# Performance work log

Hardware: AMD Instinct MI355X
Metric: run time of the kernel (lower is better)

## Reference

```python
import jax, jax.numpy as jnp
import numpy as np

NUM_HEADS = 16
HEAD_DIM = 64
HIDDEN = NUM_HEADS * HEAD_DIM  # 1024
B, S = 2, 2048
INV_NORM = 1.0 / np.sqrt(HEAD_DIM)


def setup_inputs() -> dict:
    key = jax.random.key(0)
    ks = jax.random.split(key, 8)
    hidden_states = jax.random.normal(ks[0], (1, B, S, HIDDEN), dtype=jnp.float32)
    residual = jax.random.normal(ks[1], (B, S, HIDDEN), dtype=jnp.float32)
    # ALiBi bias per (batch*head) broadcast over query positions: [B*H, 1, S]
    slopes = 2.0 ** (-8.0 * (jnp.arange(1, NUM_HEADS + 1, dtype=jnp.float32) / NUM_HEADS))
    pos = jnp.arange(S, dtype=jnp.float32)
    alibi = (slopes[:, None] * pos[None, :])[None]  # [1, H, S]
    alibi = jnp.broadcast_to(alibi, (B, NUM_HEADS, S)).reshape(B * NUM_HEADS, 1, S)
    # causal mask: True = masked out
    attention_mask = jnp.triu(jnp.ones((S, S), dtype=jnp.bool_), k=1)[None, None]  # [1,1,S,S]
    attention_mask = jnp.broadcast_to(attention_mask, (B, 1, S, S))
    W_qkv = jax.random.normal(ks[2], (3 * HIDDEN, HIDDEN), dtype=jnp.float32) * 0.02
    b_qkv = jax.random.normal(ks[3], (3 * HIDDEN,), dtype=jnp.float32) * 0.02
    W_dense = jax.random.normal(ks[4], (HIDDEN, HIDDEN), dtype=jnp.float32) * 0.02
    b_dense = jax.random.normal(ks[5], (HIDDEN,), dtype=jnp.float32) * 0.02
    return {
        "hidden_states": hidden_states,
        "residual": residual,
        "alibi": alibi,
        "attention_mask": attention_mask,
        "W_qkv": W_qkv,
        "b_qkv": b_qkv,
        "W_dense": W_dense,
        "b_dense": b_dense,
    }


def reference(hidden_states, residual, alibi, attention_mask, W_qkv, b_qkv, W_dense, b_dense):
    x = hidden_states[0]  # [B, S, H]
    b, s, _ = x.shape
    fused = x @ W_qkv.T + b_qkv  # [B, S, 3H]
    # Bloom interleaved split: [B, S, nh, 3, hd]
    qkv = fused.reshape(b, s, NUM_HEADS, 3, HEAD_DIM)
    q = jnp.transpose(qkv[..., 0, :], (0, 2, 1, 3))  # [B, nh, S, hd]
    k = jnp.transpose(qkv[..., 1, :], (0, 2, 1, 3))
    v = jnp.transpose(qkv[..., 2, :], (0, 2, 1, 3))
    # baddbmm: alibi + inv_norm * q @ k^T
    scores = jnp.einsum("bhqd,bhkd->bhqk", q, k) * INV_NORM
    scores = scores + alibi.reshape(b, NUM_HEADS, 1, s)  # [B, nh, S, S]
    neg_min = jnp.finfo(scores.dtype).min
    scores = jnp.where(attention_mask, neg_min, scores)
    probs = jax.nn.softmax(scores.astype(jnp.float32), axis=-1).astype(x.dtype)
    ctx = jnp.einsum("bhqk,bhkd->bhqd", probs, v)  # [B, nh, S, hd]
    ctx = jnp.transpose(ctx, (0, 2, 1, 3)).reshape(b, s, HIDDEN)  # merge_heads
    out = ctx @ W_dense.T + b_dense
    return out + residual  # dropout_add, eval mode
```

## Files before the change

kernel.cpp:

```cpp
#include <hip/hip_runtime.h>
#include <hip/hip_bf16.h>

#define NUM_HEADS 16
#define HEAD_DIM  64
#define HIDDEN    1024
#define BATCH     2
#define SEQ       2048
#define K_DIM     1024
#define INV_NORM  0.125f
#define LOG2E     1.4426950408889634f
#define IN2       (INV_NORM * LOG2E)

typedef __attribute__((ext_vector_type(4)))  float f32x4;
typedef __attribute__((ext_vector_type(16))) float f32x16;
typedef __attribute__((ext_vector_type(8)))  short bf16x8;
typedef __attribute__((ext_vector_type(4)))  unsigned int u32x4;
typedef __attribute__((ext_vector_type(2)))  unsigned int u32x2;
typedef unsigned short u16;

__device__ inline u16 f2bf(float f) {
    __hip_bfloat16 h = __float2bfloat16(f);
    return __builtin_bit_cast(u16, h);
}
__device__ inline float bf2f(u16 u) {
    unsigned int v = ((unsigned int)u) << 16;
    return __builtin_bit_cast(float, v);
}

__device__ inline f32x16 mfma32(bf16x8 a, bf16x8 b, f32x16 c) {
    return __builtin_amdgcn_mfma_f32_32x32x16_bf16(a, b, c, 0, 0, 0);
}

__device__ inline void gl_lds16(const u16* g, u16* s) {
    __builtin_amdgcn_global_load_lds(
        (const __attribute__((address_space(1))) unsigned int*)g,
        (__attribute__((address_space(3))) unsigned int*)s, 16, 0, 0);
}

__device__ inline void pack8(const float* src, u16* dst) {
    const float4 v0 = *reinterpret_cast<const float4*>(src);
    const float4 v1 = *reinterpret_cast<const float4*>(src + 4);
    ushort4 o0, o1;
    o0.x = f2bf(v0.x); o0.y = f2bf(v0.y); o0.z = f2bf(v0.z); o0.w = f2bf(v0.w);
    o1.x = f2bf(v1.x); o1.y = f2bf(v1.y); o1.z = f2bf(v1.z); o1.w = f2bf(v1.w);
    *reinterpret_cast<ushort4*>(dst)     = o0;
    *reinterpret_cast<ushort4*>(dst + 4) = o1;
}
__global__ __launch_bounds__(256) void cvt_all(
        const float* __restrict__ x, const float* __restrict__ wq,
        const float* __restrict__ wd,
        u16* __restrict__ xb, u16* __restrict__ wqb, u16* __restrict__ wdb) {
    int t = blockIdx.x * 256 + threadIdx.x;
    if (t < 524288) {
        int mt = t >> 12, rem = t & 4095;
        int kblk = rem >> 6, hf = (rem >> 5) & 1, ra = rem & 31;
        pack8(x + ((size_t)(mt * 32 + ra)) * K_DIM + kblk * 16 + hf * 8,
              xb + (size_t)t * 8);
    } else if (t < 917504) {
        int t2 = t - 524288;
        int nt = t2 >> 12, rem = t2 & 4095;
        int kblk = rem >> 6, hf = (rem >> 5) & 1, ra = rem & 31;
        pack8(wq + ((size_t)(nt * 32 + ra)) * K_DIM + kblk * 16 + hf * 8,
              wqb + (size_t)t2 * 8);
    } else {
        int i = (t - 917504) * 8;
        pack8(wd + i, wdb + i);
    }
}

#define QLOAD(P, kb) {                                                        \
    P##x0 = *reinterpret_cast<const bf16x8*>(pa0 + (size_t)(kb) * 512);       \
    P##x1 = *reinterpret_cast<const bf16x8*>(pa1 + (size_t)(kb) * 512);       \
    P##y0 = *reinterpret_cast<const bf16x8*>(pb0 + (size_t)(kb) * 512);       \
    P##y1 = *reinterpret_cast<const bf16x8*>(pb1 + (size_t)(kb) * 512);       \
    P##x2 = *reinterpret_cast<const bf16x8*>(pa0 + (size_t)(kb + 1) * 512);   \
    P##x3 = *reinterpret_cast<const bf16x8*>(pa1 + (size_t)(kb + 1) * 512);   \
    P##y2 = *reinterpret_cast<const bf16x8*>(pb0 + (size_t)(kb + 1) * 512);   \
    P##y3 = *reinterpret_cast<const bf16x8*>(pb1 + (size_t)(kb + 1) * 512);   \
}
#define QSTEP(P) {                                                            \
    acc[0][0] = mfma32(P##x0, P##y0, acc[0][0]);                              \
    acc[0][1] = mfma32(P##x0, P##y1, acc[0][1]);                              \
    acc[1][0] = mfma32(P##x1, P##y0, acc[1][0]);                              \
    acc[1][1] = mfma32(P##x1, P##y1, acc[1][1]);                              \
    acc[0][0] = mfma32(P##x2, P##y2, acc[0][0]);                              \
    acc[0][1] = mfma32(P##x2, P##y3, acc[0][1]);                              \
    acc[1][0] = mfma32(P##x3, P##y2, acc[1][0]);                              \
    acc[1][1] = mfma32(P##x3, P##y3, acc[1][1]);                              \
}
__global__ __launch_bounds__(256) void gemm_qkv(
        const u16* __restrict__ Af, const u16* __restrict__ Bf,
        const float* __restrict__ bias,
        u16* __restrict__ qo, u16* __restrict__ ko2, u16* __restrict__ vTo) {
    int lin = blockIdx.x;
    int g = lin & 7, i2 = lin >> 3;
    const int mblk = ((g & 3) * 8 + (i2 & 7)) * 128;
    const int nblk = ((g >> 2) * 12 + (i2 >> 3)) * 128;
    const int tid = threadIdx.x;
    const int w = tid >> 6, lane = tid & 63;
    const int la = lane & 31, hi = lane >> 5;
    const int wr = w >> 1, wc = w & 1;
    const int mt0 = (mblk >> 5) + wr * 2;
    const int nt0 = (nblk >> 5) + wc * 2;
    const u16* pa0 = Af + (size_t)mt0 * 64 * 512 + lane * 8;
    const u16* pa1 = pa0 + 64 * 512;
    const u16* pb0 = Bf + (size_t)nt0 * 64 * 512 + lane * 8;
    const u16* pb1 = pb0 + 64 * 512;
    f32x16 acc[2][2] = {};
    bf16x8 ax0, ax1, ax2, ax3, ay0, ay1, ay2, ay3;
    bf16x8 bx0, bx1, bx2, bx3, by0, by1, by2, by3;
    QLOAD(a, 0)
    #pragma unroll 4
    for (int kb = 0; kb < 64; kb += 4) {
        const int n1 = (kb + 2 < 62) ? kb + 2 : 62;
        QLOAD(b, n1)
        QSTEP(a)
        const int n2 = (kb + 4 < 62) ? kb + 4 : 62;
        QLOAD(a, n2)
        QSTEP(b)
    }
    #pragma unroll
    for (int mi = 0; mi < 2; ++mi)
    #pragma unroll
    for (int ni = 0; ni < 2; ++ni) {
        int c = nblk + wc * 64 + ni * 32 + la;
        int h = c / 192, rem = c - h * 192;
        int which = rem >> 6, d = rem & 63;
        float bv = bias[c];
        #pragma unroll
        for (int r = 0; r < 16; ++r) {
            int m = mblk + wr * 64 + mi * 32 + (r & 3) + 8 * (r >> 2) + 4 * hi;
            int bb = m >> 11, s = m & (SEQ - 1);
            int bh = bb * NUM_HEADS + h;
            int t = s >> 5;
            size_t tb = ((size_t)(bh * 64 + t)) * 2048;
            u16 o = f2bf(acc[mi][ni][r] + bv);
            if (which == 2) {
                int dblk = d >> 5, ra = d & 31;
                int k = s & 31, ks = k >> 4, hf = (k >> 3) & 1, e = k & 7;
                vTo[tb + (dblk * 2 + ks) * 512 + hf * 256 + ra * 8 + e] = o;
            } else {
                int kk = d >> 4, hf = (d >> 3) & 1, e = d & 7, ra = s & 31;
                size_t off = tb + kk * 512 + hf * 256 + ra * 8 + e;
                if (which == 0) qo[off] = o;
                else            ko2[off] = o;
            }
        }
    }
}

__global__ __launch_bounds__(256) void gemm_dense(
        const u16* __restrict__ A, const u16* __restrict__ W,
        const float* __restrict__ bias, const float* __restrict__ residual,
        float* __restrict__ out) {
    __shared__ u16 As[64 * 64];
    __shared__ u16 Bs[128 * 64];
    int lin = blockIdx.x;
    int g = lin & 7, i2 = lin >> 3;
    const int mblk = (g * 8 + (i2 & 7)) * 64;
    const int nblk = (i2 >> 3) * 128;
    const int tid = threadIdx.x;
    const int w = tid >> 6, l = tid & 63;
    const int la = l & 31, hi = l >> 5;
    const int wr = w & 1, wc = w >> 1;
    const int kperm = (((l & 7) ^ (l >> 3)) << 3);
    const u16* gA = A + (size_t)(mblk + w * 16 + (l >> 3)) * K_DIM + kperm;
    const u16* gB = W + (size_t)(nblk + w * 32 + (l >> 3)) * K_DIM + kperm;
    const int sca = (la & 7) << 3;
    f32x16 acc2[2] = {};
    for (int kt = 0; kt < 16; ++kt) {
        const int ko = kt * 64;
        gl_lds16(gA + ko,              &As[(w * 16) * 64]);
        gl_lds16(gA + ko + 8 * K_DIM,  &As[(w * 16 + 8) * 64]);
        #pragma unroll
        for (int i = 0; i < 4; ++i)
            gl_lds16(gB + i * 8 * K_DIM + ko, &Bs[(w * 32 + i * 8) * 64]);
        asm volatile("s_waitcnt vmcnt(0)" ::: "memory");
        __syncthreads();
        const u16* pA = &As[(wr * 32 + la) * 64];
        const u16* pB = &Bs[(wc * 64 + la) * 64];
        #pragma unroll
        for (int kk = 0; kk < 4; ++kk) {
            const int co = (kk * 16 + hi * 8) ^ sca;
            bf16x8 a0 = *reinterpret_cast<const bf16x8*>(pA + co);
            bf16x8 b0 = *reinterpret_cast<const bf16x8*>(pB + co);
            bf16x8 b1 = *reinterpret_cast<const bf16x8*>(pB + 32 * 64 + co);
            acc2[0] = mfma32(a0, b0, acc2[0]);
            acc2[1] = mfma32(a0, b1, acc2[1]);
        }
        __syncthreads();
    }
    #pragma unroll
    for (int ni = 0; ni < 2; ++ni) {
        int c = nblk + wc * 64 + ni * 32 + la;
        float bv = bias[c];
        #pragma unroll
        for (int r = 0; r < 16; ++r) {
            int m = mblk + wr * 32 + (r & 3) + 8 * (r >> 2) + 4 * hi;
            out[(size_t)m * HIDDEN + c] = acc2[ni][r] + bv + residual[(size_t)m * HIDDEN + c];
        }
    }
}

__global__ __launch_bounds__(256) void knorm_max(const u16* __restrict__ Kf,
                                                 float* __restrict__ kn,
                                                 unsigned int* __restrict__ ctr) {
    if (blockIdx.x == 0 && threadIdx.x < 8) ctr[threadIdx.x] = 0;
    __shared__ float red[256];
    const int bh = blockIdx.x;
    float mx = 0.f;
    for (int s = threadIdx.x; s < SEQ; s += 256) {
        const u16* kp = Kf + ((size_t)(bh * 64 + (s >> 5))) * 2048 + (s & 31) * 8;
        float ss = 0.f;
        #pragma unroll
        for (int kk = 0; kk < 4; ++kk)
        #pragma unroll
        for (int hf = 0; hf < 2; ++hf) {
            bf16x8 v = *reinterpret_cast<const bf16x8*>(kp + kk * 512 + hf * 256);
            #pragma unroll
            for (int e = 0; e < 8; ++e) {
                float f = bf2f((u16)v[e]);
                ss = fmaf(f, f, ss);
            }
        }
        mx = fmaxf(mx, ss);
    }
    red[threadIdx.x] = mx;
    __syncthreads();
    for (int off = 128; off; off >>= 1) {
        if (threadIdx.x < (unsigned)off)
            red[threadIdx.x] = fmaxf(red[threadIdx.x], red[threadIdx.x + off]);
        __syncthreads();
    }
    if (threadIdx.x == 0) kn[bh] = sqrtf(red[0]);
}

#define LOADT(P, tt) {                                                        \
    const u16* kp_ = kbase + (size_t)(tt) * 2048;                             \
    P##k0 = *reinterpret_cast<const bf16x8*>(kp_);                            \
    P##k1 = *reinterpret_cast<const bf16x8*>(kp_ + 512);                      \
    P##k2 = *reinterpret_cast<const bf16x8*>(kp_ + 1024);                     \
    P##k3 = *reinterpret_cast<const bf16x8*>(kp_ + 1536);                     \
    const u16* vp_ = vbase + (size_t)(tt) * 2048;                             \
    P##v0 = *reinterpret_cast<const bf16x8*>(vp_);                            \
    P##v1 = *reinterpret_cast<const bf16x8*>(vp_ + 512);                      \
    P##v2 = *reinterpret_cast<const bf16x8*>(vp_ + 1024);                     \
    P##v3 = *reinterpret_cast<const bf16x8*>(vp_ + 1536);                     \
}

#define STEP(P, N, tcur, tnxt, DIAG) {                                        \
    f32x16 sca_ = {}, scb_ = {};                                              \
    sca_ = mfma32(P##k0, qf0, sca_);                                          \
    scb_ = mfma32(P##k1, qf1, scb_);                                          \
    sca_ = mfma32(P##k2, qf2, sca_);                                          \
    scb_ = mfma32(P##k3, qf3, scb_);                                          \
    LOADT(N, tnxt)                                                            \
    const float Dt_ = slope2 * (float)((tcur) * 32 - qw);                     \
    float p[16];                                                              \
    _Pragma("unroll")                                                         \
    for (int r = 0; r < 16; ++r)                                              \
        p[r] = __builtin_amdgcn_exp2f(fmaf(sca_[r] + scb_[r], IN2, cl[r] + Dt_)); \
    if (DIAG) {                                                               \
        _Pragma("unroll")                                                     \
        for (int r = 0; r < 16; ++r) {                                        \
            int kr_ = (r & 3) + 8 * (r >> 2) + 4 * hi;                        \
            if (kr_ > la) p[r] = 0.f;                                         \
        }                                                                     \
    }                                                                         \
    l_i += ((p[0] + p[1]) + (p[2] + p[3])) + ((p[4] + p[5]) + (p[6] + p[7]))  \
         + ((p[8] + p[9]) + (p[10] + p[11])) + ((p[12] + p[13]) + (p[14] + p[15])); \
    unsigned pk_[8];                                                          \
    _Pragma("unroll")                                                         \
    for (int m = 0; m < 4; ++m) {                                             \
        unsigned b0_ = __builtin_bit_cast(unsigned, p[4 * m])     + 0x8000u;  \
        unsigned b1_ = __builtin_bit_cast(unsigned, p[4 * m + 1]) + 0x8000u;  \
        unsigned b2_ = __builtin_bit_cast(unsigned, p[4 * m + 2]) + 0x8000u;  \
        unsigned b3_ = __builtin_bit_cast(unsigned, p[4 * m + 3]) + 0x8000u;  \
        pk_[2 * m]     = __builtin_amdgcn_perm(b1_, b0_, 0x07060302u);        \
        pk_[2 * m + 1] = __builtin_amdgcn_perm(b3_, b2_, 0x07060302u);        \
    }                                                                         \
    u32x2 r0_ = __builtin_amdgcn_permlane32_swap(pk_[0], pk_[2], false, false); \
    u32x2 r1_ = __builtin_amdgcn_permlane32_swap(pk_[1], pk_[3], false, false); \
    u32x2 r2_ = __builtin_amdgcn_permlane32_swap(pk_[4], pk_[6], false, false); \
    u32x2 r3_ = __builtin_amdgcn_permlane32_swap(pk_[5], pk_[7], false, false); \
    u32x4 pb0_, pb1_;                                                         \
    pb0_[0] = r0_[0]; pb0_[1] = r1_[0]; pb0_[2] = r0_[1]; pb0_[3] = r1_[1];   \
    pb1_[0] = r2_[0]; pb1_[1] = r3_[0]; pb1_[2] = r2_[1]; pb1_[3] = r3_[1];   \
    bf16x8 pf0_ = __builtin_bit_cast(bf16x8, pb0_);                           \
    bf16x8 pf1_ = __builtin_bit_cast(bf16x8, pb1_);                           \
    o0 = mfma32(P##v0, pf0_, o0);                                             \
    o0 = mfma32(P##v1, pf1_, o0);                                             \
    o1 = mfma32(P##v2, pf0_, o1);                                             \
    o1 = mfma32(P##v3, pf1_, o1);                                             \
}

__global__ __launch_bounds__(256) void attn(
        const u16* __restrict__ Qf, const u16* __restrict__ Kf,
        const u16* __restrict__ Vf, const float* __restrict__ alibi,
        const float* __restrict__ kn, u16* __restrict__ ctx,
        unsigned int* __restrict__ ctr) {
    __shared__ float o_l[4][64][33];
    __shared__ float ml[4][32];
    __shared__ unsigned int s_idx;
    const int grp  = blockIdx.x & 7;
    const int lst  = grp >> 1;
    const int bat  = grp & 1;
    const unsigned long long LH = (lst == 0) ? 0x0000000007080Full
                               : (lst == 1) ? 0x000000000006090Eull
                               : (lst == 2) ? 0x0000000003050A0Dull
                                            : 0x00000102040B0Cull;
    const unsigned nit = (lst == 0) ? 192u : (lst == 3) ? 320u : 256u;
    const int wave = __builtin_amdgcn_readfirstlane(threadIdx.x >> 6);
    const int lane = threadIdx.x & 63;
    const int la = lane & 31, hi = lane >> 5;

    for (;;) {
        if (threadIdx.x == 0) s_idx = atomicAdd(ctr + grp, 1u);
        __syncthreads();
        const unsigned int idx = s_idx;
        if (idx >= nit) return;
        const int h  = (int)((LH >> (8 * (idx >> 6))) & 0xFF);
        const int qt = 63 - (int)(idx & 63);
        const int bh = bat * 16 + h;
        const int qw = qt * 32;
        const size_t tbh = (size_t)bh * 64;
        const float slope2 = alibi[(size_t)bh * SEQ + 1] * LOG2E;

        const u16* qp = Qf + (tbh + qt) * 2048 + lane * 8;
        bf16x8 qf0 = *reinterpret_cast<const bf16x8*>(qp);
        bf16x8 qf1 = *reinterpret_cast<const bf16x8*>(qp + 512);
        bf16x8 qf2 = *reinterpret_cast<const bf16x8*>(qp + 1024);
        bf16x8 qf3 = *reinterpret_cast<const bf16x8*>(qp + 1536);

        float qss = 0.f;
        #pragma unroll
        for (int e = 0; e < 8; ++e) {
            float f;
            f = bf2f((u16)qf0[e]); qss = fmaf(f, f, qss);
            f = bf2f((u16)qf1[e]); qss = fmaf(f, f, qss);
            f = bf2f((u16)qf2[e]); qss = fmaf(f, f, qss);
            f = bf2f((u16)qf3[e]); qss = fmaf(f, f, qss);
        }
        qss += __shfl_xor(qss, 32);
        float qmx = qss;
        #pragma unroll
        for (int off = 1; off <= 16; off <<= 1) qmx = fmaxf(qmx, __shfl_xor(qmx, off));
        const float kb = sqrtf(qmx) * kn[bh] * IN2;

        const float Wf = (47.f + 2.f * kb) / slope2;
        const int lo_k = qw - 31 - (int)Wf;
        const int t_lo = lo_k <= 0 ? 0 : ((lo_k + 31) >> 5);

        float cl[16];
        #pragma unroll
        for (int r = 0; r < 16; ++r)
            cl[r] = slope2 * (float)((r & 3) + 8 * (r >> 2) + 4 * hi - la) - kb;

        f32x16 o0 = {}, o1 = {};
        float l_i = 0.f;

        const int t0 = qt - wave;
        if (t0 >= t_lo) {
            const u16* kbase = Kf + tbh * 2048 + lane * 8;
            const u16* vbase = Vf + tbh * 2048 + lane * 8;
            const int nit2 = ((t0 - t_lo) >> 2) + 1;
            bf16x8 ak0, ak1, ak2, ak3, av0, av1, av2, av3;
            bf16x8 bk0, bk1, bk2, bk3, bv0, bv1, bv2, bv3;
            LOADT(a, t0)
            {
                const int tn1 = (nit2 > 1) ? t0 - 4 : t0;
                if (wave == 0) { STEP(a, b, t0, tn1, 1) }
                else           { STEP(a, b, t0, tn1, 0) }
            }
            int i = 1;
            while (i < nit2) {
                {
                    const int tc = t0 - 4 * i;
                    const int tn = (i + 1 < nit2) ? tc - 4 : tc;
                    STEP(b, a, tc, tn, 0)
                }
                ++i;
                if (i >= nit2) break;
                {
                    const int tc = t0 - 4 * i;
                    const int tn = (i + 1 < nit2) ? tc - 4 : tc;
                    STEP(a, b, tc, tn, 0)
                }
                ++i;
            }
        }

        l_i += __shfl_xor(l_i, 32);
        if (hi == 0) ml[wave][la] = l_i;
        #pragma unroll
        for (int r = 0; r < 16; ++r) {
            int d = (r & 3) + 8 * (r >> 2) + 4 * hi;
            o_l[wave][d][la]      = o0[r];
            o_l[wave][d + 32][la] = o1[r];
        }
        __syncthreads();

        const int qq = threadIdx.x >> 3;
        const int d0 = (threadIdx.x & 7) * 8;
        float L = ml[0][qq] + ml[1][qq] + ml[2][qq] + ml[3][qq];
        float inv = 1.0f / L;
        unsigned int packed[4];
        #pragma unroll
        for (int e2 = 0; e2 < 4; ++e2) {
            float Oa = o_l[0][d0 + 2 * e2][qq] + o_l[1][d0 + 2 * e2][qq]
                     + o_l[2][d0 + 2 * e2][qq] + o_l[3][d0 + 2 * e2][qq];
            float Ob = o_l[0][d0 + 2 * e2 + 1][qq] + o_l[1][d0 + 2 * e2 + 1][qq]
                     + o_l[2][d0 + 2 * e2 + 1][qq] + o_l[3][d0 + 2 * e2 + 1][qq];
            packed[e2] = (unsigned)f2bf(Oa * inv) | ((unsigned)f2bf(Ob * inv) << 16);
        }
        const int bb = bh >> 4, hh = bh & 15;
        u32x4 pv; pv[0] = packed[0]; pv[1] = packed[1]; pv[2] = packed[2]; pv[3] = packed[3];
        *reinterpret_cast<u32x4*>(
            &ctx[((size_t)(bb * SEQ + qw + qq)) * HIDDEN + hh * HEAD_DIM + d0]) = pv;
    }
}

extern "C" void kernel_launch(void* const* d_in, const int* in_sizes, int n_in,
                              void* d_out, int out_size, void* d_ws, size_t ws_size,
                              hipStream_t stream) {
    const float* x        = (const float*)d_in[0];
    const float* residual = (const float*)d_in[1];
    const float* alibi    = (const float*)d_in[2];
    const float* W_qkv    = (const float*)d_in[4];
    const float* b_qkv    = (const float*)d_in[5];
    const float* W_dense  = (const float*)d_in[6];
    const float* b_dense  = (const float*)d_in[7];
    float* out = (float*)d_out;

    char* ws = (char*)d_ws;
    u16* xb  = (u16*)(ws);
    u16* wqb = (u16*)(ws + 8388608);
    u16* wdb = (u16*)(ws + 14680064);
    u16* q   = (u16*)(ws + 16777216);
    u16* k   = (u16*)(ws + 25165824);
    u16* vT  = (u16*)(ws + 33554432);
    u16* ctx = (u16*)(ws + 41943040);
    float* kn = (float*)(ws + 50331648);
    unsigned int* ctr = (unsigned int*)(ws + 50331648 + 256);

    cvt_all<<<4096, 256, 0, stream>>>(x, W_qkv, W_dense, xb, wqb, wdb);
    gemm_qkv<<<768, 256, 0, stream>>>(xb, wqb, b_qkv, q, k, vT);
    knorm_max<<<32, 256, 0, stream>>>(k, kn, ctr);
    attn<<<1024, 256, 0, stream>>>(q, k, vT, alibi, kn, ctx, ctr);
    gemm_dense<<<512, 256, 0, stream>>>(ctx, wdb, b_dense, residual, out);
}
```

Measured before the change: 123.3 us.

## Triple-buffer K/V tile prefetch in attention and parallelize key-norm reduction

New measurement: 120.5 us. 2.3% less time.

```diff
diff --git a/kernel.cpp b/kernel.cpp
--- a/kernel.cpp
+++ b/kernel.cpp
@@ -203,36 +203,33 @@
 }
 
 __global__ __launch_bounds__(256) void knorm_max(const u16* __restrict__ Kf,
-                                                 float* __restrict__ kn,
+                                                 float* __restrict__ knp,
                                                  unsigned int* __restrict__ ctr) {
     if (blockIdx.x == 0 && threadIdx.x < 8) ctr[threadIdx.x] = 0;
     __shared__ float red[256];
-    const int bh = blockIdx.x;
-    float mx = 0.f;
-    for (int s = threadIdx.x; s < SEQ; s += 256) {
-        const u16* kp = Kf + ((size_t)(bh * 64 + (s >> 5))) * 2048 + (s & 31) * 8;
-        float ss = 0.f;
-        #pragma unroll
-        for (int kk = 0; kk < 4; ++kk)
-        #pragma unroll
-        for (int hf = 0; hf < 2; ++hf) {
-            bf16x8 v = *reinterpret_cast<const bf16x8*>(kp + kk * 512 + hf * 256);
-            #pragma unroll
-            for (int e = 0; e < 8; ++e) {
-                float f = bf2f((u16)v[e]);
-                ss = fmaf(f, f, ss);
-            }
-        }
-        mx = fmaxf(mx, ss);
-    }
-    red[threadIdx.x] = mx;
+    const int bh = blockIdx.x >> 3;
+    const int s  = (blockIdx.x & 7) * 256 + threadIdx.x;
+    const u16* kp = Kf + ((size_t)(bh * 64 + (s >> 5))) * 2048 + (s & 31) * 8;
+    float ss = 0.f;
+    #pragma unroll
+    for (int kk = 0; kk < 4; ++kk)
+    #pragma unroll
+    for (int hf = 0; hf < 2; ++hf) {
+        bf16x8 v = *reinterpret_cast<const bf16x8*>(kp + kk * 512 + hf * 256);
+        #pragma unroll
+        for (int e = 0; e < 8; ++e) {
+            float f = bf2f((u16)v[e]);
+            ss = fmaf(f, f, ss);
+        }
+    }
+    red[threadIdx.x] = ss;
     __syncthreads();
     for (int off = 128; off; off >>= 1) {
         if (threadIdx.x < (unsigned)off)
             red[threadIdx.x] = fmaxf(red[threadIdx.x], red[threadIdx.x + off]);
         __syncthreads();
     }
-    if (threadIdx.x == 0) kn[bh] = sqrtf(red[0]);
+    if (threadIdx.x == 0) knp[blockIdx.x] = sqrtf(red[0]);
 }
 
 #define LOADT(P, tt) {                                                        \
@@ -297,7 +294,7 @@
 __global__ __launch_bounds__(256) void attn(
         const u16* __restrict__ Qf, const u16* __restrict__ Kf,
         const u16* __restrict__ Vf, const float* __restrict__ alibi,
-        const float* __restrict__ kn, u16* __restrict__ ctx,
+        const float* __restrict__ knp, u16* __restrict__ ctx,
         unsigned int* __restrict__ ctr) {
     __shared__ float o_l[4][64][33];
     __shared__ float ml[4][32];
@@ -345,7 +342,10 @@
         float qmx = qss;
         #pragma unroll
         for (int off = 1; off <= 16; off <<= 1) qmx = fmaxf(qmx, __shfl_xor(qmx, off));
-        const float kb = sqrtf(qmx) * kn[bh] * IN2;
+        const float* kp8 = knp + bh * 8;
+        const float knv = fmaxf(fmaxf(fmaxf(kp8[0], kp8[1]), fmaxf(kp8[2], kp8[3])),
+                                fmaxf(fmaxf(kp8[4], kp8[5]), fmaxf(kp8[6], kp8[7])));
+        const float kb = sqrtf(qmx) * knv * IN2;
 
         const float Wf = (47.f + 2.f * kb) / slope2;
         const int lo_k = qw - 31 - (int)Wf;
@@ -364,27 +364,38 @@
             const u16* kbase = Kf + tbh * 2048 + lane * 8;
             const u16* vbase = Vf + tbh * 2048 + lane * 8;
             const int nit2 = ((t0 - t_lo) >> 2) + 1;
+            const int tlast = t0 - 4 * (nit2 - 1);
             bf16x8 ak0, ak1, ak2, ak3, av0, av1, av2, av3;
             bf16x8 bk0, bk1, bk2, bk3, bv0, bv1, bv2, bv3;
+            bf16x8 ck0, ck1, ck2, ck3, cv0, cv1, cv2, cv3;
             LOADT(a, t0)
+            const int t1 = (nit2 > 1) ? t0 - 4 : t0;
+            LOADT(b, t1)
             {
-                const int tn1 = (nit2 > 1) ? t0 - 4 : t0;
-                if (wave == 0) { STEP(a, b, t0, tn1, 1) }
-                else           { STEP(a, b, t0, tn1, 0) }
+                const int t2c = (nit2 > 2) ? t0 - 8 : tlast;
+                if (wave == 0) { STEP(a, c, t0, t2c, 1) }
+                else           { STEP(a, c, t0, t2c, 0) }
             }
             int i = 1;
             while (i < nit2) {
                 {
                     const int tc = t0 - 4 * i;
-                    const int tn = (i + 1 < nit2) ? tc - 4 : tc;
+                    const int tn = (i + 2 < nit2) ? tc - 8 : tlast;
                     STEP(b, a, tc, tn, 0)
                 }
                 ++i;
                 if (i >= nit2) break;
                 {
                     const int tc = t0 - 4 * i;
-                    const int tn = (i + 1 < nit2) ? tc - 4 : tc;
-                    STEP(a, b, tc, tn, 0)
+                    const int tn = (i + 2 < nit2) ? tc - 8 : tlast;
+                    STEP(c, b, tc, tn, 0)
+                }
+                ++i;
+                if (i >= nit2) break;
+                {
+                    const int tc = t0 - 4 * i;
+                    const int tn = (i + 2 < nit2) ? tc - 8 : tlast;
+                    STEP(a, c, tc, tn, 0)
                 }
                 ++i;
             }
@@ -440,12 +451,12 @@
     u16* k   = (u16*)(ws + 25165824);
     u16* vT  = (u16*)(ws + 33554432);
     u16* ctx = (u16*)(ws + 41943040);
-    float* kn = (float*)(ws + 50331648);
-    unsigned int* ctr = (unsigned int*)(ws + 50331648 + 256);
+    float* knp = (float*)(ws + 50331648);
+    unsigned int* ctr = (unsigned int*)(ws + 50331648 + 1024);
 
     cvt_all<<<4096, 256, 0, stream>>>(x, W_qkv, W_dense, xb, wqb, wdb);
     gemm_qkv<<<768, 256, 0, stream>>>(xb, wqb, b_qkv, q, k, vT);
-    knorm_max<<<32, 256, 0, stream>>>(k, kn, ctr);
-    attn<<<1024, 256, 0, stream>>>(q, k, vT, alibi, kn, ctx, ctr);
+    knorm_max<<<256, 256, 0, stream>>>(k, knp, ctr);
+    attn<<<1024, 256, 0, stream>>>(q, k, vT, alibi, knp, ctx, ctr);
     gemm_dense<<<512, 256, 0, stream>>>(ctx, wdb, b_dense, residual, out);
 }
```
